# Optimization experiments

Measured on AMD Instinct MI355X. Metric: run time of the kernel, lower is better.

Reference implementation:

```python
import jax, jax.numpy as jnp
import numpy as np

VOCAB, EMB, RNN, OUT = 32000, 512, 1024, 4


def setup_inputs() -> dict:
    key = jax.random.key(0)
    ks = jax.random.split(key, 8)
    stdv = 1.0 / np.sqrt(RNN)
    u = lambda k, shape, s: jax.random.uniform(k, shape, jnp.float32, -s, s)
    return {
        "x": jax.random.randint(ks[0], (512, 64), 0, VOCAB),
        "emb_table": jax.random.normal(ks[1], (VOCAB, EMB), jnp.float32),
        "w_ih": u(ks[2], (3 * RNN, EMB), stdv),
        "w_hh": u(ks[3], (3 * RNN, RNN), stdv),
        "b_ih": u(ks[4], (3 * RNN,), stdv),
        "b_hh": u(ks[5], (3 * RNN,), stdv),
        "fc_w": u(ks[6], (OUT, RNN), 1.0 / np.sqrt(RNN)),
        "fc_b": u(ks[7], (OUT,), 1.0 / np.sqrt(RNN)),
    }


def reference(x, emb_table, w_ih, w_hh, b_ih, b_hh, fc_w, fc_b):
    # x: [T, B] int indices
    T, B = x.shape
    embedded = emb_table[x]  # [T, B, EMB]
    # precompute input projections for all timesteps at once: [T, B, 3*RNN]
    gi_all = jnp.einsum('tbe,ge->tbg', embedded, w_ih) + b_ih

    def step(h, gi):
        gh = h @ w_hh.T + b_hh  # [B, 3*RNN]
        i_r, i_i, i_n = jnp.split(gi, 3, axis=1)
        h_r, h_i, h_n = jnp.split(gh, 3, axis=1)
        r = jax.nn.sigmoid(i_r + h_r)
        z = jax.nn.sigmoid(i_i + h_i)
        n = jnp.tanh(i_n + r * h_n)
        hy = z * n + (1.0 - z) * h  # note: matches GRUCellExposed (z gates newgate)
        return hy, hy

    h0 = jnp.zeros((B, w_hh.shape[1]), embedded.dtype)
    h_last, _ = jax.lax.scan(step, h0, gi_all)
    out = h_last @ fc_w.T + fc_b  # [B, OUT]
    return out
```

## Files before the change

### kernel.cpp

```cpp
#include <hip/hip_runtime.h>
#include <hip/hip_bf16.h>

typedef __attribute__((ext_vector_type(8))) short  short8;
typedef __attribute__((ext_vector_type(4))) float  f32x4;

#define T_TOTAL 512
#define BATCH   64
#define VOCAB   32000
#define EMB     512
#define RNN     1024
#define G3      3072
#define WROWS   48
#define WPAD    1032
#define APAD2   520
#define RPAD    18
#define NWG     256
#define NGRP    4
#define NLINE   2
#define REC_SMEM (WROWS * WPAD * 2 + WROWS * APAD2 * 2 + 4 * WROWS * RPAD * 4)

__device__ __forceinline__ unsigned short f2bf(float f) {
    union { float f; unsigned int u; } v; v.f = f;
    unsigned int r = v.u + 0x7fffu + ((v.u >> 16) & 1u);
    return (unsigned short)(r >> 16);
}
__device__ __forceinline__ float bf2f(unsigned short h) {
    union { unsigned int u; float f; } v; v.u = ((unsigned int)h) << 16;
    return v.f;
}
__device__ __forceinline__ float sigmoidf_(float x) { return 1.f / (1.f + __expf(-x)); }
__device__ __forceinline__ float tanhf_(float x) {
    float ax = fabsf(x);
    float e2 = __expf(-2.f * ax);
    float t  = (1.f - e2) / (1.f + e2);
    return x < 0.f ? -t : t;
}

__device__ __forceinline__ void gbar_arrive(unsigned int* lines, int lid,
                                            unsigned int ph) {
    __syncthreads();
    if (threadIdx.x == 0)
        __hip_atomic_fetch_add(&lines[lid * 64], 1u,
                               __ATOMIC_RELAXED, __HIP_MEMORY_SCOPE_AGENT);
}
__device__ __forceinline__ void gbar_wait(unsigned int* lines, unsigned int ph) {
    if (threadIdx.x < NLINE) {
        while (__hip_atomic_load(&lines[threadIdx.x * 64], __ATOMIC_RELAXED,
                                 __HIP_MEMORY_SCOPE_AGENT) < ph * 32u)
            __builtin_amdgcn_s_sleep(1);
    }
    __syncthreads();
}

__global__ void bar_init(unsigned int* bar) {
    for (int i = threadIdx.x; i < NGRP * 256; i += 256) bar[i] = 0;
}

__global__ __launch_bounds__(256) void cvt_bf16_kernel(
    const float* __restrict__ s, unsigned short* __restrict__ d, int n8)
{
    const int i = blockIdx.x * 256 + threadIdx.x;
    if (i >= n8) return;
    const float4 a = ((const float4*)s)[i * 2];
    const float4 b = ((const float4*)s)[i * 2 + 1];
    short8 v;
    v[0] = f2bf(a.x); v[1] = f2bf(a.y); v[2] = f2bf(a.z); v[3] = f2bf(a.w);
    v[4] = f2bf(b.x); v[5] = f2bf(b.y); v[6] = f2bf(b.z); v[7] = f2bf(b.w);
    ((short8*)d)[i] = v;
}

template<bool BF>
__global__ __launch_bounds__(256, 1) void rec_kernel(
    const int* __restrict__ x, const void* __restrict__ embp,
    const float* __restrict__ w_ih, const float* __restrict__ b_ih,
    const float* __restrict__ w_hh, const float* __restrict__ b_hh,
    unsigned short* __restrict__ hb0, unsigned short* __restrict__ hb1,
    float* __restrict__ hf, unsigned int* bar, int t0, int nsteps, int pbase)
{
    extern __shared__ __align__(16) char smem[];
    unsigned short* Wsm = (unsigned short*)smem;
    unsigned short* Wih = (unsigned short*)smem + WROWS * WPAD;
    float (*red)[WROWS][RPAD] =
        (float (*)[WROWS][RPAD])(smem + WROWS * WPAD * 2 + WROWS * APAD2 * 2);

    const int tid = threadIdx.x;
    const int wg  = blockIdx.x;
    const int grp = wg & 3, sidx = wg >> 2;
    const int b0 = grp * 16, j0 = sidx * 16;
    unsigned int* lines = &bar[grp * 256];
    const int lid = sidx & (NLINE - 1);

    #pragma unroll 4
    for (int it = 0; it < 48; ++it) {
        const int i   = it * 256 + tid;
        const int row = i >> 8;
        const int c4  = (i & 255) * 4;
        const int gate = row >> 4, uu = row & 15;
        const float4 v = *(const float4*)(w_hh + (size_t)(gate * RNN + j0 + uu) * RNN + c4);
        unsigned short* dst = &Wsm[row * WPAD + c4];
        dst[0] = f2bf(v.x); dst[1] = f2bf(v.y); dst[2] = f2bf(v.z); dst[3] = f2bf(v.w);
    }
    #pragma unroll 4
    for (int it = 0; it < 24; ++it) {
        const int i   = it * 256 + tid;
        const int row = i >> 7;
        const int c4  = (i & 127) * 4;
        const int gate = row >> 4, uu = row & 15;
        const float4 v = *(const float4*)(w_ih + (size_t)(gate * RNN + j0 + uu) * EMB + c4);
        unsigned short* dst = &Wih[row * APAD2 + c4];
        dst[0] = f2bf(v.x); dst[1] = f2bf(v.y); dst[2] = f2bf(v.z); dst[3] = f2bf(v.w);
    }

    const int u  = tid & 15;
    const int bl = tid >> 4;
    const int j  = j0 + u;
    const int b  = b0 + bl;
    const float bhr  = b_hh[j], bhi  = b_hh[RNN + j], bhn  = b_hh[2 * RNN + j];
    const float bihr = b_ih[j], bihi = b_ih[RNN + j], bihn = b_ih[2 * RNN + j];

    float h_reg;
    if (t0 == 0) {
        h_reg = 0.f;
        if ((u & 1) == 0)
            __hip_atomic_store((unsigned int*)&hb0[b * RNN + j], 0u,
                               __ATOMIC_RELAXED, __HIP_MEMORY_SCOPE_AGENT);
    } else {
        h_reg = hf[b * RNN + j];
    }
    gbar_arrive(lines, lid, (unsigned)(pbase + 1));

    const int lane = tid & 63, kq = tid >> 6;
    const int lr = lane & 15, lq = lane >> 4;
    const unsigned short* wbase  = Wsm + kq * 256 + lq * 8;
    const unsigned short* wibase = Wih + kq * 128 + lq * 8;
    const size_t hoff = ((size_t)(b0 + lr) * RNN + kq * 256 + lq * 8) >> 2;

    auto gi_compute = [&](int tg) {
        const int xi = x[tg * BATCH + b0 + lr];
        short8 bfr[4];
        if constexpr (BF) {
            const unsigned short* erow = (const unsigned short*)embp
                                       + (size_t)xi * EMB + kq * 128 + lq * 8;
            #pragma unroll
            for (int ks = 0; ks < 4; ++ks)
                bfr[ks] = *(const short8*)(erow + ks * 32);
        } else {
            const float* erow = (const float*)embp
                              + (size_t)xi * EMB + kq * 128 + lq * 8;
            #pragma unroll
            for (int ks = 0; ks < 4; ++ks) {
                const float4 e0 = *(const float4*)(erow + ks * 32);
                const float4 e1 = *(const float4*)(erow + ks * 32 + 4);
                short8 v;
                v[0]=f2bf(e0.x); v[1]=f2bf(e0.y); v[2]=f2bf(e0.z); v[3]=f2bf(e0.w);
                v[4]=f2bf(e1.x); v[5]=f2bf(e1.y); v[6]=f2bf(e1.z); v[7]=f2bf(e1.w);
                bfr[ks] = v;
            }
        }
        f32x4 acc2[3];
        acc2[0] = (f32x4){0.f, 0.f, 0.f, 0.f};
        acc2[1] = (f32x4){0.f, 0.f, 0.f, 0.f};
        acc2[2] = (f32x4){0.f, 0.f, 0.f, 0.f};
        #pragma unroll
        for (int ks = 0; ks < 4; ++ks)
            #pragma unroll
            for (int gt = 0; gt < 3; ++gt) {
                const short8 a = *(const short8*)(wibase + (gt * 16 + lr) * APAD2 + ks * 32);
                acc2[gt] = __builtin_amdgcn_mfma_f32_16x16x32_bf16(a, bfr[ks],
                                                                   acc2[gt], 0, 0, 0);
            }
        #pragma unroll
        for (int gt = 0; gt < 3; ++gt)
            #pragma unroll
            for (int q = 0; q < 4; ++q)
                red[kq][gt * 16 + lq * 4 + q][lr] = acc2[gt][q];
    };

    gi_compute(t0);
    gbar_wait(lines, (unsigned)(pbase + 1));

    for (int t = 0; t < nsteps; ++t) {
        const float gir = red[0][u][bl]      + red[1][u][bl]
                        + red[2][u][bl]      + red[3][u][bl]      + bihr;
        const float gii = red[0][16 + u][bl] + red[1][16 + u][bl]
                        + red[2][16 + u][bl] + red[3][16 + u][bl] + bihi;
        const float gin = red[0][32 + u][bl] + red[1][32 + u][bl]
                        + red[2][32 + u][bl] + red[3][32 + u][bl] + bihn;

        const unsigned short* hrd = (t & 1) ? hb1 : hb0;
        unsigned short*       hwr = (t & 1) ? hb0 : hb1;

        union { unsigned long long q[2]; short8 s8; } hv[8];
        const unsigned long long* hp = (const unsigned long long*)hrd + hoff;
        #pragma unroll
        for (int ks = 0; ks < 8; ++ks) {
            hv[ks].q[0] = __hip_atomic_load(hp + ks * 8,     __ATOMIC_RELAXED,
                                            __HIP_MEMORY_SCOPE_AGENT);
            hv[ks].q[1] = __hip_atomic_load(hp + ks * 8 + 1, __ATOMIC_RELAXED,
                                            __HIP_MEMORY_SCOPE_AGENT);
        }

        f32x4 acc[3];
        acc[0] = (f32x4){0.f, 0.f, 0.f, 0.f};
        acc[1] = (f32x4){0.f, 0.f, 0.f, 0.f};
        acc[2] = (f32x4){0.f, 0.f, 0.f, 0.f};
        #pragma unroll
        for (int ks = 0; ks < 8; ++ks) {
            const int k = ks * 32;
            #pragma unroll
            for (int gt = 0; gt < 3; ++gt) {
                const short8 a = *(const short8*)(wbase + (gt * 16 + lr) * WPAD + k);
                acc[gt] = __builtin_amdgcn_mfma_f32_16x16x32_bf16(a, hv[ks].s8,
                                                                  acc[gt], 0, 0, 0);
            }
        }
        __syncthreads();
        #pragma unroll
        for (int gt = 0; gt < 3; ++gt)
            #pragma unroll
            for (int q = 0; q < 4; ++q)
                red[kq][gt * 16 + lq * 4 + q][lr] = acc[gt][q];
        __syncthreads();

        const float ghr = red[0][u][bl]      + red[1][u][bl]
                        + red[2][u][bl]      + red[3][u][bl];
        const float ghi = red[0][16 + u][bl] + red[1][16 + u][bl]
                        + red[2][16 + u][bl] + red[3][16 + u][bl];
        const float ghn = red[0][32 + u][bl] + red[1][32 + u][bl]
                        + red[2][32 + u][bl] + red[3][32 + u][bl];
        const float rr = sigmoidf_(gir + ghr + bhr);
        const float zz = sigmoidf_(gii + ghi + bhi);
        const float nn = tanhf_(gin + rr * (ghn + bhn));
        h_reg = zz * nn + (1.f - zz) * h_reg;

        unsigned int hvv = (unsigned int)f2bf(h_reg);
        unsigned int ovv = __shfl_xor((int)hvv, 1);
        if ((u & 1) == 0)
            __hip_atomic_store((unsigned int*)&hwr[b * RNN + j],
                               hvv | (ovv << 16), __ATOMIC_RELAXED,
                               __HIP_MEMORY_SCOPE_AGENT);

        gbar_arrive(lines, lid, (unsigned)(pbase + 2 + t));
        const int tn = (t + 1 < nsteps) ? t + 1 : t;
        gi_compute(t0 + tn);
        gbar_wait(lines, (unsigned)(pbase + 2 + t));
    }
    hf[b * RNN + j] = h_reg;
}

__global__ __launch_bounds__(256) void out_kernel(
    const float* __restrict__ hf, const float* __restrict__ fc_w,
    const float* __restrict__ fc_b, float* __restrict__ out)
{
    __shared__ float red[256];
    const int bidx = blockIdx.x, tid = threadIdx.x;
    const int o = tid & 3, seg = tid >> 2;
    const float* hp = hf   + (size_t)bidx * RNN + seg * 16;
    const float* wp = fc_w + (size_t)o * RNN + seg * 16;
    float acc = 0.f;
    #pragma unroll
    for (int i = 0; i < 16; ++i) acc += hp[i] * wp[i];
    red[tid] = acc;
    __syncthreads();
    if (tid < 4) {
        float sv = fc_b[tid];
        #pragma unroll 8
        for (int q = 0; q < 64; ++q) sv += red[q * 4 + tid];
        out[bidx * 4 + tid] = sv;
    }
}

extern "C" void kernel_launch(void* const* d_in, const int* in_sizes, int n_in,
                              void* d_out, int out_size, void* d_ws, size_t ws_size,
                              hipStream_t stream)
{
    const int*   x     = (const int*)d_in[0];
    const float* emb   = (const float*)d_in[1];
    const float* w_ih  = (const float*)d_in[2];
    const float* w_hh  = (const float*)d_in[3];
    const float* b_ih  = (const float*)d_in[4];
    const float* b_hh  = (const float*)d_in[5];
    const float* fc_w  = (const float*)d_in[6];
    const float* fc_b  = (const float*)d_in[7];
    float*       out   = (float*)d_out;

    const size_t bar_b   = (size_t)NGRP * 256 * 4;
    const size_t base_b  = 2 * (size_t)BATCH * RNN * 2
                         + (size_t)BATCH * RNN * 4 + bar_b;
    const size_t embbf_b = (size_t)VOCAB * EMB * 2;
    const bool bfpath = ws_size >= base_b + embbf_b;

    char* ws = (char*)d_ws;
    size_t off = 0;
    unsigned short* hb0 = (unsigned short*)(ws + off); off += (size_t)BATCH * RNN * 2;
    unsigned short* hb1 = (unsigned short*)(ws + off); off += (size_t)BATCH * RNN * 2;
    float*          hf  = (float*)(ws + off);          off += (size_t)BATCH * RNN * 4;
    unsigned int*   bar = (unsigned int*)(ws + off);   off += bar_b;
    unsigned short* embbf = (unsigned short*)(ws + off);

    hipFuncSetAttribute((const void*)rec_kernel<true>,
                        hipFuncAttributeMaxDynamicSharedMemorySize, REC_SMEM);
    hipFuncSetAttribute((const void*)rec_kernel<false>,
                        hipFuncAttributeMaxDynamicSharedMemorySize, REC_SMEM);

    bar_init<<<dim3(1), dim3(256), 0, stream>>>(bar);
    if (bfpath)
        cvt_bf16_kernel<<<dim3((VOCAB * EMB / 8 + 255) / 256), dim3(256), 0, stream>>>(
            emb, embbf, VOCAB * EMB / 8);

    int t0 = 0, ns = T_TOTAL, pb = 0;
    const void* embp = bfpath ? (const void*)embbf : (const void*)emb;
    void* args[13];
    args[0]  = (void*)&x;    args[1]  = (void*)&embp;  args[2]  = (void*)&w_ih;
    args[3]  = (void*)&b_ih; args[4]  = (void*)&w_hh;  args[5]  = (void*)&b_hh;
    args[6]  = (void*)&hb0;  args[7]  = (void*)&hb1;   args[8]  = (void*)&hf;
    args[9]  = (void*)&bar;  args[10] = (void*)&t0;    args[11] = (void*)&ns;
    args[12] = (void*)&pb;
    if (bfpath)
        hipLaunchCooperativeKernel((const void*)rec_kernel<true>, dim3(NWG), dim3(256),
                                   args, REC_SMEM, stream);
    else
        hipLaunchCooperativeKernel((const void*)rec_kernel<false>, dim3(NWG), dim3(256),
                                   args, REC_SMEM, stream);
    out_kernel<<<dim3(BATCH), dim3(256), 0, stream>>>(hf, fc_w, fc_b, out);
}
```

Measured before the change: 2.227 ms.

## Keep W_ih fragments in registers and prefetch next-step embeddings early

The input-projection weight slice moves out of LDS and into per-thread register fragments (12 short8 per thread), so the gi MFMAs no longer read it from shared memory each step. The embedding gather for the next timestep is also split out and issued right after the h loads, ahead of the recurrent MFMAs, so its global latency can overlap that work instead of sitting between barrier arrive and wait. This frees LDS but raises register pressure, which could cause spills in a kernel with one workgroup per CU.

Result: faster. 1.916 ms (-14.0%).

```diff
diff --git a/kernel.cpp b/kernel.cpp
--- a/kernel.cpp
+++ b/kernel.cpp
@@ -12,12 +12,11 @@
 #define G3      3072
 #define WROWS   48
 #define WPAD    1032
-#define APAD2   520
 #define RPAD    18
 #define NWG     256
 #define NGRP    4
 #define NLINE   2
-#define REC_SMEM (WROWS * WPAD * 2 + WROWS * APAD2 * 2 + 4 * WROWS * RPAD * 4)
+#define REC_SMEM (WROWS * WPAD * 2 + 4 * WROWS * RPAD * 4)
 
 __device__ __forceinline__ unsigned short f2bf(float f) {
     union { float f; unsigned int u; } v; v.f = f;
@@ -79,9 +78,7 @@
 {
     extern __shared__ __align__(16) char smem[];
     unsigned short* Wsm = (unsigned short*)smem;
-    unsigned short* Wih = (unsigned short*)smem + WROWS * WPAD;
-    float (*red)[WROWS][RPAD] =
-        (float (*)[WROWS][RPAD])(smem + WROWS * WPAD * 2 + WROWS * APAD2 * 2);
+    float (*red)[WROWS][RPAD] = (float (*)[WROWS][RPAD])(smem + WROWS * WPAD * 2);
 
     const int tid = threadIdx.x;
     const int wg  = blockIdx.x;
@@ -100,15 +97,24 @@
         unsigned short* dst = &Wsm[row * WPAD + c4];
         dst[0] = f2bf(v.x); dst[1] = f2bf(v.y); dst[2] = f2bf(v.z); dst[3] = f2bf(v.w);
     }
-    #pragma unroll 4
-    for (int it = 0; it < 24; ++it) {
-        const int i   = it * 256 + tid;
-        const int row = i >> 7;
-        const int c4  = (i & 127) * 4;
-        const int gate = row >> 4, uu = row & 15;
-        const float4 v = *(const float4*)(w_ih + (size_t)(gate * RNN + j0 + uu) * EMB + c4);
-        unsigned short* dst = &Wih[row * APAD2 + c4];
-        dst[0] = f2bf(v.x); dst[1] = f2bf(v.y); dst[2] = f2bf(v.z); dst[3] = f2bf(v.w);
+
+    const int lane = tid & 63, kq = tid >> 6;
+    const int lr = lane & 15, lq = lane >> 4;
+
+    short8 wihf[3][4];
+    #pragma unroll
+    for (int gt = 0; gt < 3; ++gt) {
+        const float* srow = w_ih + (size_t)(gt * RNN + j0 + lr) * EMB
+                          + kq * 128 + lq * 8;
+        #pragma unroll
+        for (int ks = 0; ks < 4; ++ks) {
+            const float4 s0 = *(const float4*)(srow + ks * 32);
+            const float4 s1 = *(const float4*)(srow + ks * 32 + 4);
+            short8 w;
+            w[0]=f2bf(s0.x); w[1]=f2bf(s0.y); w[2]=f2bf(s0.z); w[3]=f2bf(s0.w);
+            w[4]=f2bf(s1.x); w[5]=f2bf(s1.y); w[6]=f2bf(s1.z); w[7]=f2bf(s1.w);
+            wihf[gt][ks] = w;
+        }
     }
 
     const int u  = tid & 15;
@@ -129,15 +135,11 @@
     }
     gbar_arrive(lines, lid, (unsigned)(pbase + 1));
 
-    const int lane = tid & 63, kq = tid >> 6;
-    const int lr = lane & 15, lq = lane >> 4;
-    const unsigned short* wbase  = Wsm + kq * 256 + lq * 8;
-    const unsigned short* wibase = Wih + kq * 128 + lq * 8;
+    const unsigned short* wbase = Wsm + kq * 256 + lq * 8;
     const size_t hoff = ((size_t)(b0 + lr) * RNN + kq * 256 + lq * 8) >> 2;
 
-    auto gi_compute = [&](int tg) {
+    auto gi_load = [&](int tg, short8* bfr) {
         const int xi = x[tg * BATCH + b0 + lr];
-        short8 bfr[4];
         if constexpr (BF) {
             const unsigned short* erow = (const unsigned short*)embp
                                        + (size_t)xi * EMB + kq * 128 + lq * 8;
@@ -157,6 +159,8 @@
                 bfr[ks] = v;
             }
         }
+    };
+    auto gi_mfma = [&](const short8* bfr) {
         f32x4 acc2[3];
         acc2[0] = (f32x4){0.f, 0.f, 0.f, 0.f};
         acc2[1] = (f32x4){0.f, 0.f, 0.f, 0.f};
@@ -164,11 +168,9 @@
         #pragma unroll
         for (int ks = 0; ks < 4; ++ks)
             #pragma unroll
-            for (int gt = 0; gt < 3; ++gt) {
-                const short8 a = *(const short8*)(wibase + (gt * 16 + lr) * APAD2 + ks * 32);
-                acc2[gt] = __builtin_amdgcn_mfma_f32_16x16x32_bf16(a, bfr[ks],
-                                                                   acc2[gt], 0, 0, 0);
-            }
+            for (int gt = 0; gt < 3; ++gt)
+                acc2[gt] = __builtin_amdgcn_mfma_f32_16x16x32_bf16(
+                    wihf[gt][ks], bfr[ks], acc2[gt], 0, 0, 0);
         #pragma unroll
         for (int gt = 0; gt < 3; ++gt)
             #pragma unroll
@@ -176,7 +178,9 @@
                 red[kq][gt * 16 + lq * 4 + q][lr] = acc2[gt][q];
     };
 
-    gi_compute(t0);
+    short8 bfr[4];
+    gi_load(t0, bfr);
+    gi_mfma(bfr);
     gbar_wait(lines, (unsigned)(pbase + 1));
 
     for (int t = 0; t < nsteps; ++t) {
@@ -199,6 +203,8 @@
             hv[ks].q[1] = __hip_atomic_load(hp + ks * 8 + 1, __ATOMIC_RELAXED,
                                             __HIP_MEMORY_SCOPE_AGENT);
         }
+        const int tn = (t + 1 < nsteps) ? t + 1 : t;
+        gi_load(t0 + tn, bfr);
 
         f32x4 acc[3];
         acc[0] = (f32x4){0.f, 0.f, 0.f, 0.f};
@@ -241,8 +247,7 @@
                                __HIP_MEMORY_SCOPE_AGENT);
 
         gbar_arrive(lines, lid, (unsigned)(pbase + 2 + t));
-        const int tn = (t + 1 < nsteps) ? t + 1 : t;
-        gi_compute(t0 + tn);
+        gi_mfma(bfr);
         gbar_wait(lines, (unsigned)(pbase + 2 + t));
     }
     hf[b * RNN + j] = h_reg;
```
